# Kernel tuning notes

Hardware: AMD Instinct MI355X
Metric: run time of the kernel (lower is better)

## Reference

```python
import jax, jax.numpy as jnp
import numpy as np

N_NODES = 100000
N_EDGES = 1600000
IN_CH = 128
HID = 128
OUT_CH = 10
NUM_LAYERS = 3
NUM_GRAPHS = 512


def _glorot(key, shape):
    fan_in, fan_out = shape[0], shape[1]
    lim = jnp.sqrt(6.0 / (fan_in + fan_out))
    return jax.random.uniform(key, shape, jnp.float32, -lim, lim)


def setup_inputs() -> dict:
    key = jax.random.key(0)
    ks = jax.random.split(key, 20)
    inp = {}
    inp["x"] = jax.random.normal(ks[0], (N_NODES, IN_CH), jnp.float32)
    inp["edge_index"] = jax.random.randint(ks[1], (2, N_EDGES), 0, N_NODES, jnp.int64)
    inp["batch"] = jnp.sort(jax.random.randint(ks[2], (N_NODES,), 0, NUM_GRAPHS, jnp.int64))
    # GIN layer MLP params: Linear(in, hid) -> ReLU -> Linear(hid, hid)
    kidx = 3
    for l in range(NUM_LAYERS):
        d_in = IN_CH if l == 0 else HID
        inp[f"w1_{l}"] = _glorot(ks[kidx], (d_in, HID)); kidx += 1
        inp[f"b1_{l}"] = jnp.zeros((HID,), jnp.float32)
        inp[f"w2_{l}"] = _glorot(ks[kidx], (HID, HID)); kidx += 1
        inp[f"b2_{l}"] = jnp.zeros((HID,), jnp.float32)
    inp["lin_w"] = _glorot(ks[kidx], (HID, OUT_CH))
    inp["lin_b"] = jnp.zeros((OUT_CH,), jnp.float32)
    return inp


def _gin_forward(x, src, dst, batch, layer_params, lin_w, lin_b):
    h = x
    n_layers = len(layer_params)
    for i, (w1, b1, w2, b2) in enumerate(layer_params):
        # GINConv: (1 + eps) * h + sum_{j in N(i)} h_j, eps = 0
        agg = jax.ops.segment_sum(h[src], dst, num_segments=N_NODES)
        z = h + agg
        # MLP: Linear -> ReLU -> Linear
        h = jnp.maximum(z @ w1 + b1, 0.0) @ w2 + b2
        if i < n_layers - 1:  # inter-layer ReLU (PyG BasicGNN act)
            h = jnp.maximum(h, 0.0)
    # global_add_pool over batch ids -> [NUM_GRAPHS, HID]
    pooled = jax.ops.segment_sum(h, batch, num_segments=NUM_GRAPHS)
    # dropout(p=0.5) is identity in eval mode
    return pooled @ lin_w + lin_b


def reference(x, edge_index, batch,
              w1_0, b1_0, w2_0, b2_0,
              w1_1, b1_1, w2_1, b2_1,
              w1_2, b1_2, w2_2, b2_2,
              lin_w, lin_b):
    src, dst = edge_index[0], edge_index[1]
    layer_params = [(w1_0, b1_0, w2_0, b2_0),
                    (w1_1, b1_1, w2_1, b2_1),
                    (w1_2, b1_2, w2_2, b2_2)]
    return _gin_forward(x, src, dst, batch, layer_params, lin_w, lin_b)
```

## Files before the change

kernel.cpp:

```cpp
#include <hip/hip_runtime.h>

#define CH 128
#define OUTC 10
#define NB 256
#define BCAP 10240
#define PCHUNK 2048
#define PQ2 132
#define FBM 64

typedef __attribute__((ext_vector_type(8))) short short8;
typedef __attribute__((ext_vector_type(4))) short short4v;
typedef __attribute__((ext_vector_type(16))) float f32x16;
typedef __attribute__((ext_vector_type(2))) float f32x2;


__device__ inline unsigned short f2bf(float f) {
    unsigned u = __builtin_bit_cast(unsigned, f);
    u += 0x7fffu + ((u >> 16) & 1u);
    return (unsigned short)(u >> 16);
}
__device__ inline float bflo(unsigned u) { return __builtin_bit_cast(float, u << 16); }
__device__ inline float bfhi(unsigned u) { return __builtin_bit_cast(float, u & 0xffff0000u); }

__device__ inline f32x2 bf2(unsigned u) {
    return (f32x2){__builtin_bit_cast(float, u << 16),
                   __builtin_bit_cast(float, u & 0xffff0000u)};
}

__device__ inline void acc8(f32x2* a, const uint4& v) {
    a[0] += bf2(v.x);
    a[1] += bf2(v.y);
    a[2] += bf2(v.z);
    a[3] += bf2(v.w);
}


struct WPtrs { const float* s[6]; unsigned short* d[6]; };

__global__ void prep_part_kernel(const int* __restrict__ src, const int* __restrict__ dst,
                                 int* __restrict__ bucketCnt, unsigned* __restrict__ pairs, int E,
                                 int nPartBlk,
                                 const float4* __restrict__ x4, uint2* __restrict__ xb, int n4,
                                 int nConvBlk, WPtrs p,
                                 uint4* __restrict__ pooled4, int nPooled4) {
    __shared__ int hist[NB];
    __shared__ int base[NB];
    __shared__ int cur[NB];
    int tid = threadIdx.x;
    int b = blockIdx.x;

    if (b < nPartBlk) {
        int e0 = b * PCHUNK;
        hist[tid] = 0;
        __syncthreads();
        #pragma unroll
        for (int i = 0; i < PCHUNK / 256; ++i) {
            int e = e0 + tid + i * 256;
            if (e < E) atomicAdd(&hist[dst[e] >> 9], 1);
        }
        __syncthreads();
        {
            int c = hist[tid];
            base[tid] = (c > 0) ? atomicAdd(&bucketCnt[tid], c) : 0;
            cur[tid] = 0;
        }
        __syncthreads();
        #pragma unroll
        for (int i = 0; i < PCHUNK / 256; ++i) {
            int e = e0 + tid + i * 256;
            if (e < E) {
                int d = dst[e];
                int bkt = d >> 9;
                int pos = base[bkt] + atomicAdd(&cur[bkt], 1);
                if (pos < BCAP)
                    pairs[bkt * BCAP + pos] = ((unsigned)(d & 511) << 17) | (unsigned)src[e];
            }
        }
    } else if (b < nPartBlk + nConvBlk) {
        int i = (b - nPartBlk) * 256 + tid;
        if (i < n4) {
            float4 v = x4[i];
            uint2 o;
            o.x = (unsigned)f2bf(v.x) | ((unsigned)f2bf(v.y) << 16);
            o.y = (unsigned)f2bf(v.z) | ((unsigned)f2bf(v.w) << 16);
            xb[i] = o;
        }
    } else if (b < nPartBlk + nConvBlk + 384) {
        int bb = b - nPartBlk - nConvBlk;
        int m = bb >> 6;
        int i = (bb & 63) * 256 + tid;
        int j = i & 7;
        int l = (i >> 3) & 63;
        int k0 = (i >> 9) & 7;
        int ct = (i >> 12) & 3;
        int k = k0 * 16 + ((l >> 5) << 3) + j;
        int nn = ct * 32 + (l & 31);
        p.d[m][i] = f2bf(p.s[m][k * CH + nn]);
    } else {
        int i = (b - nPartBlk - nConvBlk - 384) * 256 + tid;
        if (i < nPooled4) pooled4[i] = make_uint4(0, 0, 0, 0);
    }
}


__launch_bounds__(512)
__global__ void build_csr_kernel(const unsigned* __restrict__ pairs, const int* __restrict__ bucketCnt,
                                 int* __restrict__ offs, int* __restrict__ csr, int N) {
    __shared__ int bsm[NB];
    __shared__ int ldeg[512];
    __shared__ int s0[512], s1[512];
    __shared__ int lexc[512];
    __shared__ int lcur[512];
    __shared__ int lcsr[BCAP];

    int b = blockIdx.x;
    int node0 = b << 9;
    if (node0 >= N) return;
    int nLocal = min(512, N - node0);
    int tid = threadIdx.x;

    if (tid < NB) bsm[tid] = bucketCnt[tid];
    __syncthreads();
    for (int off = 1; off < NB; off <<= 1) {
        int t = 0;
        if (tid < NB) t = (tid >= off) ? bsm[tid - off] : 0;
        __syncthreads();
        if (tid < NB) bsm[tid] += t;
        __syncthreads();
    }
    int cnt = min(bucketCnt[b], BCAP);
    int gbase = bsm[b] - bucketCnt[b];

    ldeg[tid] = 0;
    __syncthreads();
    for (int i = tid; i < cnt; i += 512)
        atomicAdd(&ldeg[pairs[b * BCAP + i] >> 17], 1);
    __syncthreads();

    s0[tid] = ldeg[tid];
    __syncthreads();
    int* sp = s0; int* dp = s1;
    for (int off = 1; off < 512; off <<= 1) {
        dp[tid] = sp[tid] + ((tid >= off) ? sp[tid - off] : 0);
        __syncthreads();
        int* t = sp; sp = dp; dp = t;
    }
    {
        int ex = sp[tid] - ldeg[tid];
        lexc[tid] = ex;
        lcur[tid] = ex;
    }
    __syncthreads();

    for (int i = tid; i < cnt; i += 512) {
        unsigned w = pairs[b * BCAP + i];
        int ppos = atomicAdd(&lcur[w >> 17], 1);
        lcsr[ppos] = (int)(w & 0x1ffffu);
    }
    __syncthreads();

    for (int i = tid; i < cnt; i += 512) csr[gbase + i] = lcsr[i];
    for (int i = tid; i < nLocal; i += 512) offs[node0 + i] = gbase + lexc[i];
    if (tid == 0 && node0 + nLocal == N) offs[N] = gbase + cnt;
}


template <int L, int RELU, int POOL>
__launch_bounds__(512)
__global__ void fused_gin_kernel(const uint4* __restrict__ h4,
                                 const int* __restrict__ offs, const int* __restrict__ csr,
                                 const unsigned short* __restrict__ w1s, const float* __restrict__ b1,
                                 const unsigned short* __restrict__ w2s, const float* __restrict__ b2,
                                 unsigned short* __restrict__ hout,
                                 const int* __restrict__ batch, float* __restrict__ pooled,
                                 int n) {
    __shared__ __align__(16) unsigned short zs[FBM * PQ2];

    int tid = threadIdx.x;
    int row0 = blockIdx.x * FBM;

    {
        int gl = tid & 7;
        int grp = tid >> 3;
        int g2 = gl * 2;
        int node = row0 + grp;
        unsigned o0 = 0, o1 = 0, o2 = 0, o3 = 0, o4 = 0, o5 = 0, o6 = 0, o7 = 0;
        if (node < n) {
            int beg = offs[node], end = offs[node + 1];
            f32x2 a[8];
            {
                uint4 sa = h4[node * 16 + g2];
                uint4 sb = h4[node * 16 + g2 + 1];
                a[0] = bf2(sa.x); a[1] = bf2(sa.y); a[2] = bf2(sa.z); a[3] = bf2(sa.w);
                a[4] = bf2(sb.x); a[5] = bf2(sb.y); a[6] = bf2(sb.z); a[7] = bf2(sb.w);
            }
            int e = beg;
            for (; e + 4 <= end; e += 4) {
                int i0 = csr[e], i1 = csr[e + 1], i2 = csr[e + 2], i3 = csr[e + 3];
                uint4 v0a = h4[i0 * 16 + g2], v0b = h4[i0 * 16 + g2 + 1];
                uint4 v1a = h4[i1 * 16 + g2], v1b = h4[i1 * 16 + g2 + 1];
                uint4 v2a = h4[i2 * 16 + g2], v2b = h4[i2 * 16 + g2 + 1];
                uint4 v3a = h4[i3 * 16 + g2], v3b = h4[i3 * 16 + g2 + 1];
                acc8(a, v0a); acc8(a + 4, v0b);
                acc8(a, v1a); acc8(a + 4, v1b);
                acc8(a, v2a); acc8(a + 4, v2b);
                acc8(a, v3a); acc8(a + 4, v3b);
            }
            for (; e < end; ++e) {
                int i0 = csr[e];
                uint4 va = h4[i0 * 16 + g2], vb = h4[i0 * 16 + g2 + 1];
                acc8(a, va); acc8(a + 4, vb);
            }
            o0 = (unsigned)f2bf(a[0][0]) | ((unsigned)f2bf(a[0][1]) << 16);
            o1 = (unsigned)f2bf(a[1][0]) | ((unsigned)f2bf(a[1][1]) << 16);
            o2 = (unsigned)f2bf(a[2][0]) | ((unsigned)f2bf(a[2][1]) << 16);
            o3 = (unsigned)f2bf(a[3][0]) | ((unsigned)f2bf(a[3][1]) << 16);
            o4 = (unsigned)f2bf(a[4][0]) | ((unsigned)f2bf(a[4][1]) << 16);
            o5 = (unsigned)f2bf(a[5][0]) | ((unsigned)f2bf(a[5][1]) << 16);
            o6 = (unsigned)f2bf(a[6][0]) | ((unsigned)f2bf(a[6][1]) << 16);
            o7 = (unsigned)f2bf(a[7][0]) | ((unsigned)f2bf(a[7][1]) << 16);
        }
        *(uint2*)&zs[grp * PQ2 + gl * 16]      = make_uint2(o0, o1);
        *(uint2*)&zs[grp * PQ2 + gl * 16 + 4]  = make_uint2(o2, o3);
        *(uint2*)&zs[grp * PQ2 + gl * 16 + 8]  = make_uint2(o4, o5);
        *(uint2*)&zs[grp * PQ2 + gl * 16 + 12] = make_uint2(o6, o7);
    }
    __syncthreads();

    int wv = tid >> 6;
    int lane = tid & 63;
    int l31 = lane & 31;
    int kh = lane >> 5;
    int rt = wv & 1;
    int ct = wv >> 1;
    int arow = rt * 32 + l31;

    f32x16 acc;
    {
        float bv = b1[ct * 32 + l31];
        #pragma unroll
        for (int r = 0; r < 16; ++r) acc[r] = bv;
    }
    #pragma unroll
    for (int k0 = 0; k0 < 8; ++k0) {
        short8 afr;
        {
            short4v lo = *(const short4v*)&zs[arow * PQ2 + k0 * 16 + kh * 8];
            short4v hi = *(const short4v*)&zs[arow * PQ2 + k0 * 16 + kh * 8 + 4];
            afr = (short8){lo[0], lo[1], lo[2], lo[3], hi[0], hi[1], hi[2], hi[3]};
        }
        short8 bfr = *(const short8*)&w1s[(((ct * 8 + k0) * 64) + lane) * 8];
        acc = __builtin_amdgcn_mfma_f32_32x32x16_bf16(afr, bfr, acc, 0, 0, 0);
    }
    __syncthreads();

    #pragma unroll
    for (int reg = 0; reg < 16; ++reg) {
        int crow = (reg & 3) + 8 * (reg >> 2) + 4 * kh;
        zs[(rt * 32 + crow) * PQ2 + ct * 32 + l31] = f2bf(fmaxf(acc[reg], 0.f));
    }
    __syncthreads();

    {
        float bv = b2[ct * 32 + l31];
        #pragma unroll
        for (int r = 0; r < 16; ++r) acc[r] = bv;
    }
    #pragma unroll
    for (int k0 = 0; k0 < 8; ++k0) {
        short8 afr;
        {
            short4v lo = *(const short4v*)&zs[arow * PQ2 + k0 * 16 + kh * 8];
            short4v hi = *(const short4v*)&zs[arow * PQ2 + k0 * 16 + kh * 8 + 4];
            afr = (short8){lo[0], lo[1], lo[2], lo[3], hi[0], hi[1], hi[2], hi[3]};
        }
        short8 bfr = *(const short8*)&w2s[(((ct * 8 + k0) * 64) + lane) * 8];
        acc = __builtin_amdgcn_mfma_f32_32x32x16_bf16(afr, bfr, acc, 0, 0, 0);
    }
    __syncthreads();

    #pragma unroll
    for (int reg = 0; reg < 16; ++reg) {
        int crow = (reg & 3) + 8 * (reg >> 2) + 4 * kh;
        float v = acc[reg];
        if (RELU) v = fmaxf(v, 0.f);
        zs[(rt * 32 + crow) * PQ2 + ct * 32 + l31] = f2bf(v);
    }
    __syncthreads();

    if (!POOL) {
        for (int i = tid; i < FBM * 16; i += 512) {
            int r = i >> 4, c = i & 15;
            int row = row0 + r;
            if (row < n) {
                uint2 a2 = *(const uint2*)&zs[r * PQ2 + c * 8];
                uint2 b2v = *(const uint2*)&zs[r * PQ2 + c * 8 + 4];
                ((uint4*)hout)[row * 16 + c] = make_uint4(a2.x, a2.y, b2v.x, b2v.y);
            }
        }
    } else {
        int c2 = tid & 63;
        int rs = tid >> 6;
        float a0 = 0.f, a1 = 0.f;
        int prevg = -1;
        #pragma unroll
        for (int i = 0; i < FBM / 8; ++i) {
            int r = rs + 8 * i;
            int row = row0 + r;
            if (row >= n) break;
            int g = batch[row];
            if (g != prevg) {
                if (prevg >= 0) {
                    atomicAdd(&pooled[prevg * CH + 2 * c2], a0);
                    atomicAdd(&pooled[prevg * CH + 2 * c2 + 1], a1);
                }
                prevg = g; a0 = 0.f; a1 = 0.f;
            }
            unsigned v = *(const unsigned*)&zs[r * PQ2 + c2 * 2];
            a0 += bflo(v); a1 += bfhi(v);
        }
        if (prevg >= 0) {
            atomicAdd(&pooled[prevg * CH + 2 * c2], a0);
            atomicAdd(&pooled[prevg * CH + 2 * c2 + 1], a1);
        }
    }
}


__global__ void final_linear_kernel(const float* __restrict__ pooled, const float* __restrict__ lin_w,
                                    const float* __restrict__ lin_b, float* __restrict__ out) {
    int g = blockIdx.x;
    int tid = threadIdx.x;
    __shared__ float pl[CH];
    pl[tid] = pooled[g * CH + tid];
    __syncthreads();
    if (tid < OUTC) {
        float a = lin_b[tid];
        #pragma unroll 16
        for (int c = 0; c < CH; ++c) a = fmaf(pl[c], lin_w[c * OUTC + tid], a);
        out[g * OUTC + tid] = a;
    }
}


static inline size_t aln(size_t x) { return (x + 255) & ~size_t(255); }

extern "C" void kernel_launch(void* const* d_in, const int* in_sizes, int n_in,
                              void* d_out, int out_size, void* d_ws, size_t ws_size,
                              hipStream_t stream) {
    const float* x      = (const float*)d_in[0];
    const int*   ei     = (const int*)d_in[1];
    const int*   batch  = (const int*)d_in[2];
    const float* w1[3]  = {(const float*)d_in[3], (const float*)d_in[7],  (const float*)d_in[11]};
    const float* b1[3]  = {(const float*)d_in[4], (const float*)d_in[8],  (const float*)d_in[12]};
    const float* w2[3]  = {(const float*)d_in[5], (const float*)d_in[9],  (const float*)d_in[13]};
    const float* b2[3]  = {(const float*)d_in[6], (const float*)d_in[10], (const float*)d_in[14]};
    const float* lin_w  = (const float*)d_in[15];
    const float* lin_b  = (const float*)d_in[16];
    float* out = (float*)d_out;

    int E = in_sizes[1] / 2;
    int N = in_sizes[2];
    int n_graphs = out_size / OUTC;
    const int* src = ei;
    const int* dst = ei + E;

    char* p = (char*)d_ws;
    int* bucketCnt  = (int*)p; p += aln(NB * 4);
    unsigned* pairs = (unsigned*)p; p += aln((size_t)NB * BCAP * 4);
    int* offs       = (int*)p; p += aln((size_t)(N + 1) * 4);
    int* csr        = (int*)p; p += aln((size_t)E * 4);
    unsigned short* xb = (unsigned short*)p; p += aln((size_t)N * CH * 2);
    unsigned short* hA = (unsigned short*)p; p += aln((size_t)N * CH * 2);
    unsigned short* hB = (unsigned short*)p; p += aln((size_t)N * CH * 2);
    float* pooled = (float*)p; p += aln((size_t)n_graphs * CH * 4);
    unsigned short* wt[6];
    for (int i = 0; i < 6; ++i) { wt[i] = (unsigned short*)p; p += aln((size_t)CH * CH * 2); }
    (void)ws_size; (void)n_in;

    hipMemsetAsync(bucketCnt, 0, NB * 4, stream);

    int n4 = N * CH / 4;
    int nConvBlk = (n4 + 255) / 256;
    int nPartBlk = (E + PCHUNK - 1) / PCHUNK;
    int nPooled4 = n_graphs * CH / 4;
    int nZeroBlk = (nPooled4 + 255) / 256;
    WPtrs wp;
    for (int l = 0; l < 3; ++l) {
        wp.s[2 * l] = w1[l];     wp.d[2 * l] = wt[2 * l];
        wp.s[2 * l + 1] = w2[l]; wp.d[2 * l + 1] = wt[2 * l + 1];
    }
    prep_part_kernel<<<nPartBlk + nConvBlk + 384 + nZeroBlk, 256, 0, stream>>>(
        src, dst, bucketCnt, pairs, E, nPartBlk,
        (const float4*)x, (uint2*)xb, n4, nConvBlk, wp,
        (uint4*)pooled, nPooled4);

    build_csr_kernel<<<NB, 512, 0, stream>>>(pairs, bucketCnt, offs, csr, N);

    int fblk = (N + FBM - 1) / FBM;

    fused_gin_kernel<0, 1, 0><<<fblk, 512, 0, stream>>>((const uint4*)xb, offs, csr,
        wt[0], b1[0], wt[1], b2[0], hA, batch, pooled, N);
    fused_gin_kernel<1, 1, 0><<<fblk, 512, 0, stream>>>((const uint4*)hA, offs, csr,
        wt[2], b1[1], wt[3], b2[1], hB, batch, pooled, N);
    fused_gin_kernel<2, 0, 1><<<fblk, 512, 0, stream>>>((const uint4*)hB, offs, csr,
        wt[4], b1[2], wt[5], b2[2], (unsigned short*)nullptr, batch, pooled, N);

    final_linear_kernel<<<n_graphs, CH, 0, stream>>>(pooled, lin_w, lin_b, out);
}
```

Before: 397.3 us.

## Split fused GIN layer into column-quarter gather kernel and separate MLP kernel

Each layer's fused gather+MLP kernel is replaced by two kernels. The first gathers neighbor sums into a global bf16 buffer, with each block handling one quarter of the channels for a tile of nodes; blocks are ordered so that the same channel quarter is processed for consecutive node tiles, which is meant to improve cache locality of the random row reads. The second kernel reads the aggregated tile from global memory and runs the MLP. The cost is an extra round trip of N*128 bf16 values through global memory per layer, extra kernel launches, and four separate index/offset reads per node.

```diff
diff --git a/kernel.cpp b/kernel.cpp
--- a/kernel.cpp
+++ b/kernel.cpp
@@ -27,11 +27,9 @@
                    __builtin_bit_cast(float, u & 0xffff0000u)};
 }
 
-__device__ inline void acc8(f32x2* a, const uint4& v) {
+__device__ inline void acc4(f32x2* a, const uint2& v) {
     a[0] += bf2(v.x);
     a[1] += bf2(v.y);
-    a[2] += bf2(v.z);
-    a[3] += bf2(v.w);
 }
 
 
@@ -165,65 +163,65 @@
 }
 
 
-template <int L, int RELU, int POOL>
 __launch_bounds__(512)
-__global__ void fused_gin_kernel(const uint4* __restrict__ h4,
-                                 const int* __restrict__ offs, const int* __restrict__ csr,
-                                 const unsigned short* __restrict__ w1s, const float* __restrict__ b1,
-                                 const unsigned short* __restrict__ w2s, const float* __restrict__ b2,
-                                 unsigned short* __restrict__ hout,
-                                 const int* __restrict__ batch, float* __restrict__ pooled,
-                                 int n) {
+__global__ void gather_q_kernel(const uint2* __restrict__ h2,
+                                const int* __restrict__ offs, const int* __restrict__ csr,
+                                uint2* __restrict__ z2, int n) {
+    int b = blockIdx.x;
+    int r = b & 7;
+    int quarter = r >> 1;
+    int dstBlk = (b >> 3) * 2 + (r & 1);
+    int gl = threadIdx.x & 7;
+    int grp = threadIdx.x >> 3;
+    int node = dstBlk * FBM + grp;
+    if (node >= n) return;
+    int cb = quarter * 8 + gl;
+
+    int beg = offs[node], end = offs[node + 1];
+    f32x2 a[2];
+    {
+        uint2 s = h2[node * 32 + cb];
+        a[0] = bf2(s.x); a[1] = bf2(s.y);
+    }
+    int e = beg;
+    for (; e + 4 <= end; e += 4) {
+        int i0 = csr[e], i1 = csr[e + 1], i2 = csr[e + 2], i3 = csr[e + 3];
+        uint2 v0 = h2[i0 * 32 + cb];
+        uint2 v1 = h2[i1 * 32 + cb];
+        uint2 v2 = h2[i2 * 32 + cb];
+        uint2 v3 = h2[i3 * 32 + cb];
+        acc4(a, v0); acc4(a, v1); acc4(a, v2); acc4(a, v3);
+    }
+    for (; e < end; ++e) {
+        uint2 v = h2[csr[e] * 32 + cb];
+        acc4(a, v);
+    }
+    uint2 o;
+    o.x = (unsigned)f2bf(a[0][0]) | ((unsigned)f2bf(a[0][1]) << 16);
+    o.y = (unsigned)f2bf(a[1][0]) | ((unsigned)f2bf(a[1][1]) << 16);
+    z2[node * 32 + cb] = o;
+}
+
+
+template <int RELU, int POOL>
+__launch_bounds__(512)
+__global__ void mlp_kernel(const uint2* __restrict__ z2g,
+                           const unsigned short* __restrict__ w1s, const float* __restrict__ b1,
+                           const unsigned short* __restrict__ w2s, const float* __restrict__ b2,
+                           unsigned short* __restrict__ hout,
+                           const int* __restrict__ batch, float* __restrict__ pooled,
+                           int n) {
     __shared__ __align__(16) unsigned short zs[FBM * PQ2];
 
     int tid = threadIdx.x;
     int row0 = blockIdx.x * FBM;
 
-    {
-        int gl = tid & 7;
-        int grp = tid >> 3;
-        int g2 = gl * 2;
-        int node = row0 + grp;
-        unsigned o0 = 0, o1 = 0, o2 = 0, o3 = 0, o4 = 0, o5 = 0, o6 = 0, o7 = 0;
-        if (node < n) {
-            int beg = offs[node], end = offs[node + 1];
-            f32x2 a[8];
-            {
-                uint4 sa = h4[node * 16 + g2];
-                uint4 sb = h4[node * 16 + g2 + 1];
-                a[0] = bf2(sa.x); a[1] = bf2(sa.y); a[2] = bf2(sa.z); a[3] = bf2(sa.w);
-                a[4] = bf2(sb.x); a[5] = bf2(sb.y); a[6] = bf2(sb.z); a[7] = bf2(sb.w);
-            }
-            int e = beg;
-            for (; e + 4 <= end; e += 4) {
-                int i0 = csr[e], i1 = csr[e + 1], i2 = csr[e + 2], i3 = csr[e + 3];
-                uint4 v0a = h4[i0 * 16 + g2], v0b = h4[i0 * 16 + g2 + 1];
-                uint4 v1a = h4[i1 * 16 + g2], v1b = h4[i1 * 16 + g2 + 1];
-                uint4 v2a = h4[i2 * 16 + g2], v2b = h4[i2 * 16 + g2 + 1];
-                uint4 v3a = h4[i3 * 16 + g2], v3b = h4[i3 * 16 + g2 + 1];
-                acc8(a, v0a); acc8(a + 4, v0b);
-                acc8(a, v1a); acc8(a + 4, v1b);
-                acc8(a, v2a); acc8(a + 4, v2b);
-                acc8(a, v3a); acc8(a + 4, v3b);
-            }
-            for (; e < end; ++e) {
-                int i0 = csr[e];
-                uint4 va = h4[i0 * 16 + g2], vb = h4[i0 * 16 + g2 + 1];
-                acc8(a, va); acc8(a + 4, vb);
-            }
-            o0 = (unsigned)f2bf(a[0][0]) | ((unsigned)f2bf(a[0][1]) << 16);
-            o1 = (unsigned)f2bf(a[1][0]) | ((unsigned)f2bf(a[1][1]) << 16);
-            o2 = (unsigned)f2bf(a[2][0]) | ((unsigned)f2bf(a[2][1]) << 16);
-            o3 = (unsigned)f2bf(a[3][0]) | ((unsigned)f2bf(a[3][1]) << 16);
-            o4 = (unsigned)f2bf(a[4][0]) | ((unsigned)f2bf(a[4][1]) << 16);
-            o5 = (unsigned)f2bf(a[5][0]) | ((unsigned)f2bf(a[5][1]) << 16);
-            o6 = (unsigned)f2bf(a[6][0]) | ((unsigned)f2bf(a[6][1]) << 16);
-            o7 = (unsigned)f2bf(a[7][0]) | ((unsigned)f2bf(a[7][1]) << 16);
-        }
-        *(uint2*)&zs[grp * PQ2 + gl * 16]      = make_uint2(o0, o1);
-        *(uint2*)&zs[grp * PQ2 + gl * 16 + 4]  = make_uint2(o2, o3);
-        *(uint2*)&zs[grp * PQ2 + gl * 16 + 8]  = make_uint2(o4, o5);
-        *(uint2*)&zs[grp * PQ2 + gl * 16 + 12] = make_uint2(o6, o7);
+    for (int i = tid; i < FBM * 32; i += 512) {
+        int rr = i >> 5, cc = i & 31;
+        int row = row0 + rr;
+        uint2 v = make_uint2(0, 0);
+        if (row < n) v = z2g[row * 32 + cc];
+        *(uint2*)&zs[rr * PQ2 + cc * 4] = v;
     }
     __syncthreads();
 
@@ -373,6 +371,7 @@
     unsigned short* xb = (unsigned short*)p; p += aln((size_t)N * CH * 2);
     unsigned short* hA = (unsigned short*)p; p += aln((size_t)N * CH * 2);
     unsigned short* hB = (unsigned short*)p; p += aln((size_t)N * CH * 2);
+    unsigned short* zb = (unsigned short*)p; p += aln((size_t)N * CH * 2);
     float* pooled = (float*)p; p += aln((size_t)n_graphs * CH * 4);
     unsigned short* wt[6];
     for (int i = 0; i < 6; ++i) { wt[i] = (unsigned short*)p; p += aln((size_t)CH * CH * 2); }
@@ -398,13 +397,25 @@
     build_csr_kernel<<<NB, 512, 0, stream>>>(pairs, bucketCnt, offs, csr, N);
 
     int fblk = (N + FBM - 1) / FBM;
-
-    fused_gin_kernel<0, 1, 0><<<fblk, 512, 0, stream>>>((const uint4*)xb, offs, csr,
-        wt[0], b1[0], wt[1], b2[0], hA, batch, pooled, N);
-    fused_gin_kernel<1, 1, 0><<<fblk, 512, 0, stream>>>((const uint4*)hA, offs, csr,
-        wt[2], b1[1], wt[3], b2[1], hB, batch, pooled, N);
-    fused_gin_kernel<2, 0, 1><<<fblk, 512, 0, stream>>>((const uint4*)hB, offs, csr,
-        wt[4], b1[2], wt[5], b2[2], (unsigned short*)nullptr, batch, pooled, N);
+    int nPair = (fblk + 1) / 2;
+    int gblk = nPair * 8;
+
+    const unsigned short* hin[3] = {xb, hA, hB};
+    unsigned short* hout[3] = {hA, hB, nullptr};
+
+    for (int l = 0; l < 3; ++l) {
+        gather_q_kernel<<<gblk, 512, 0, stream>>>(
+            (const uint2*)hin[l], offs, csr, (uint2*)zb, N);
+        if (l < 2) {
+            mlp_kernel<1, 0><<<fblk, 512, 0, stream>>>(
+                (const uint2*)zb, wt[2 * l], b1[l], wt[2 * l + 1], b2[l],
+                hout[l], batch, pooled, N);
+        } else {
+            mlp_kernel<0, 1><<<fblk, 512, 0, stream>>>(
+                (const uint2*)zb, wt[2 * l], b1[l], wt[2 * l + 1], b2[l],
+                nullptr, batch, pooled, N);
+        }
+    }
 
     final_linear_kernel<<<n_graphs, CH, 0, stream>>>(pooled, lin_w, lin_b, out);
 }
```

New measurement: 530.6 us. 33.5% more time.
